# Kernel tuning notes

Measured on AMD Instinct MI355X. Metric: run time of the kernel, lower is better.

## Reference

```python
import jax, jax.numpy as jnp
import numpy as np

TEMPERATURE = 0.07
N, D, NUM_CLASSES = 8192, 1024, 128


def setup_inputs() -> dict:
    key = jax.random.key(0)
    k1, k2 = jax.random.split(key)
    embeddings = jax.random.normal(k1, (N, D), dtype=jnp.float32)
    labels = jax.random.randint(k2, (N,), 0, NUM_CLASSES, dtype=jnp.int64)
    return {"embeddings": embeddings, "labels": labels}


def reference(embeddings, labels):
    # L2-normalize rows (eps matches F.normalize default clamp of 1e-12 on the norm)
    norm = jnp.maximum(jnp.linalg.norm(embeddings, axis=-1, keepdims=True), 1e-12)
    emb = embeddings / norm
    # [N, N] similarity scaled by temperature
    sim = jnp.matmul(emb, emb.T) / TEMPERATURE
    # positive mask: same label, diagonal zeroed
    pos_mask = (labels[:, None] == labels[None, :]).astype(sim.dtype)
    pos_mask = pos_mask * (1.0 - jnp.eye(sim.shape[0], dtype=sim.dtype))
    exp_sim = jnp.exp(sim)
    sum_exp = exp_sim.sum(axis=1)              # [N]
    pos_sum = (exp_sim * pos_mask).sum(axis=1)  # [N]
    loss = -jnp.log(pos_sum / sum_exp)
    return loss.mean()
```

## Files before the change

kernel.cpp:

```cpp
#include <hip/hip_runtime.h>
#include <hip/hip_bf16.h>
#include <math.h>

#define N 8192
#define D 1024
#define TILE 128
#define BK 32
#define NTILES (N / TILE)
#define NBLOCKS (NTILES * (NTILES + 1) / 2)

typedef __bf16 bf16_t;
typedef bf16_t bf16x4 __attribute__((ext_vector_type(4)));
typedef bf16_t bf16x8 __attribute__((ext_vector_type(8)));
typedef float f32x4 __attribute__((ext_vector_type(4)));

__global__ __launch_bounds__(256) void norm_cast(const float* __restrict__ in,
                                                 bf16_t* __restrict__ out) {
    const int row = blockIdx.x;
    const int tid = threadIdx.x;
    const float4 v = ((const float4*)(in + (size_t)row * D))[tid];
    float ss = v.x * v.x + v.y * v.y + v.z * v.z + v.w * v.w;
    #pragma unroll
    for (int off = 32; off >= 1; off >>= 1) ss += __shfl_xor(ss, off, 64);
    __shared__ float red[4];
    const int wave = tid >> 6, lane = tid & 63;
    if (lane == 0) red[wave] = ss;
    __syncthreads();
    const float tot = red[0] + red[1] + red[2] + red[3];
    const float scale = 1.0f / fmaxf(sqrtf(tot), 1e-12f);
    bf16x4 o;
    o[0] = (bf16_t)(v.x * scale);
    o[1] = (bf16_t)(v.y * scale);
    o[2] = (bf16_t)(v.z * scale);
    o[3] = (bf16_t)(v.w * scale);
    ((bf16x4*)(out + (size_t)row * D))[tid] = o;
}

__global__ __launch_bounds__(256) void gemm_fused(const bf16_t* __restrict__ E,
                                                  const int* __restrict__ labels,
                                                  float* __restrict__ sumExp,
                                                  float* __restrict__ posSum) {
    __shared__ bf16_t As[TILE * BK];
    __shared__ bf16_t Bs[TILE * BK];
    __shared__ int labR[TILE], labC[TILE];

    const int b = blockIdx.x;
    int ti = (int)((sqrtf(8.0f * (float)b + 1.0f) - 1.0f) * 0.5f);
    while ((ti + 1) * (ti + 2) / 2 <= b) ++ti;
    while (ti * (ti + 1) / 2 > b) --ti;
    const int tj = b - ti * (ti + 1) / 2;
    const bool isDiag = (ti == tj);

    const int tid     = threadIdx.x;
    const int wave    = tid >> 6;
    const int lane    = tid & 63;
    const int q       = lane >> 4;
    const int lr      = lane & 15;
    const int waveRow = wave >> 1;
    const int waveCol = wave & 1;
    const int rowStart = ti * TILE;
    const int colStart = tj * TILE;

    if (tid < TILE) labR[tid] = labels[rowStart + tid];
    else            labC[tid - TILE] = labels[colStart + (tid - TILE)];

    f32x4 acc[4][4];
    #pragma unroll
    for (int i = 0; i < 4; ++i)
        #pragma unroll
        for (int j = 0; j < 4; ++j)
            acc[i][j] = {0.f, 0.f, 0.f, 0.f};

    const char* baseA = (const char*)(E + (size_t)rowStart * D);
    const char* baseB = (const char*)(E + (size_t)colStart * D);

    const int runit = q ^ ((lr >> 1) & 3);

    for (int kk = 0; kk < D; kk += BK) {
        #pragma unroll
        for (int p = 0; p < 2; ++p) {
            const int u  = p * 256 + tid;
            const int r  = u >> 2;
            const int uc = (u & 3) ^ ((r >> 1) & 3);
            const char* ga = baseA + (size_t)r * (D * 2) + kk * 2 + uc * 16;
            const char* gb = baseB + (size_t)r * (D * 2) + kk * 2 + uc * 16;
            char* la = (char*)As + (p * 256 + wave * 64) * 16;
            char* lb = (char*)Bs + (p * 256 + wave * 64) * 16;
            __builtin_amdgcn_global_load_lds(
                (const __attribute__((address_space(1))) void*)ga,
                (__attribute__((address_space(3))) void*)la, 16, 0, 0);
            __builtin_amdgcn_global_load_lds(
                (const __attribute__((address_space(1))) void*)gb,
                (__attribute__((address_space(3))) void*)lb, 16, 0, 0);
        }
        __syncthreads();

        bf16x8 af[4], bfr[4];
        #pragma unroll
        for (int ri = 0; ri < 4; ++ri)
            af[ri] = *(const bf16x8*)((const char*)As +
                     (waveRow * 64 + ri * 16 + lr) * 64 + runit * 16);
        #pragma unroll
        for (int ci = 0; ci < 4; ++ci)
            bfr[ci] = *(const bf16x8*)((const char*)Bs +
                      (waveCol * 64 + ci * 16 + lr) * 64 + runit * 16);
        #pragma unroll
        for (int ri = 0; ri < 4; ++ri)
            #pragma unroll
            for (int ci = 0; ci < 4; ++ci)
                acc[ri][ci] = __builtin_amdgcn_mfma_f32_16x16x32_bf16(
                    af[ri], bfr[ci], acc[ri][ci], 0, 0, 0);
        __syncthreads();
    }

    const float invT = 1.0f / 0.07f;
    float colAll[4] = {0.f, 0.f, 0.f, 0.f};
    float colPos[4] = {0.f, 0.f, 0.f, 0.f};
    #pragma unroll
    for (int ri = 0; ri < 4; ++ri) {
        #pragma unroll
        for (int e = 0; e < 4; ++e) {
            const int rloc = waveRow * 64 + ri * 16 + q * 4 + e;
            const int gi   = rowStart + rloc;
            const int li   = labR[rloc];
            float s_all = 0.f, s_pos = 0.f;
            #pragma unroll
            for (int ci = 0; ci < 4; ++ci) {
                const int cloc = waveCol * 64 + ci * 16 + lr;
                const int gj   = colStart + cloc;
                const float v  = __expf(acc[ri][ci][e] * invT);
                const bool same = (labC[cloc] == li);
                s_all += v;
                if (same && gi != gj) s_pos += v;
                if (!isDiag) {
                    colAll[ci] += v;
                    if (same) colPos[ci] += v;
                }
            }
            #pragma unroll
            for (int off = 1; off < 16; off <<= 1) {
                s_all += __shfl_xor(s_all, off, 64);
                s_pos += __shfl_xor(s_pos, off, 64);
            }
            if (lr == 0) {
                atomicAdd(&sumExp[gi], s_all);
                atomicAdd(&posSum[gi], s_pos);
            }
        }
    }
    if (!isDiag) {
        #pragma unroll
        for (int ci = 0; ci < 4; ++ci) {
            float a = colAll[ci], p = colPos[ci];
            a += __shfl_xor(a, 16, 64);  a += __shfl_xor(a, 32, 64);
            p += __shfl_xor(p, 16, 64);  p += __shfl_xor(p, 32, 64);
            if (q == 0) {
                const int gj = colStart + waveCol * 64 + ci * 16 + lr;
                atomicAdd(&sumExp[gj], a);
                atomicAdd(&posSum[gj], p);
            }
        }
    }
}

__global__ __launch_bounds__(1024) void finalize(const float* __restrict__ sumExp,
                                                 const float* __restrict__ posSum,
                                                 float* __restrict__ out) {
    const int tid = threadIdx.x;
    float s = 0.f;
    #pragma unroll
    for (int i = tid; i < N; i += 1024)
        s += __logf(sumExp[i] / posSum[i]);
    #pragma unroll
    for (int off = 32; off >= 1; off >>= 1) s += __shfl_xor(s, off, 64);
    __shared__ float red[16];
    if ((tid & 63) == 0) red[tid >> 6] = s;
    __syncthreads();
    if (tid == 0) {
        float t = 0.f;
        #pragma unroll
        for (int i = 0; i < 16; ++i) t += red[i];
        out[0] = t / (float)N;
    }
}

extern "C" void kernel_launch(void* const* d_in, const int* in_sizes, int n_in,
                              void* d_out, int out_size, void* d_ws, size_t ws_size,
                              hipStream_t stream) {
    const float* emb    = (const float*)d_in[0];
    const int*   labels = (const int*)d_in[1];
    float* out = (float*)d_out;

    float*  sumExp = (float*)d_ws;
    float*  posSum = sumExp + N;
    bf16_t* EN     = (bf16_t*)((char*)d_ws + (size_t)2 * N * sizeof(float));

    hipMemsetAsync(d_ws, 0, (size_t)2 * N * sizeof(float), stream);

    norm_cast<<<N, 256, 0, stream>>>(emb, EN);

    gemm_fused<<<NBLOCKS, 256, 0, stream>>>(EN, labels, sumExp, posSum);

    finalize<<<1, 1024, 0, stream>>>(sumExp, posSum, out);
}
```

Measured before the change: 216.6 us.

## Rewrite fused GEMM with 256x256 tiles, double-buffered async LDS staging and phased MFMA schedule

The fused similarity GEMM moves from 128x128 tiles with a single-buffered BK=32 loop to 256x256 tiles with 512 threads and BK=64 double-buffered LDS. Global-to-LDS loads are interleaved with MFMA phases using explicit waitcnt, barriers and setprio, so that memory latency overlaps compute. Block indices are remapped in strides of 8 to spread tiles across the device. Labels are now read straight from global memory instead of through shared memory. The larger tiles raise data reuse, but they also raise register and LDS pressure, and 528 blocks may balance less evenly across the CUs.

```diff
diff --git a/kernel.cpp b/kernel.cpp
--- a/kernel.cpp
+++ b/kernel.cpp
@@ -4,10 +4,11 @@
 
 #define N 8192
 #define D 1024
-#define TILE 128
-#define BK 32
-#define NTILES (N / TILE)
-#define NBLOCKS (NTILES * (NTILES + 1) / 2)
+#define BM 256
+#define BK 64
+#define NTIL 32
+#define NBLK 528
+#define ITERS 8
 
 typedef __bf16 bf16_t;
 typedef bf16_t bf16x4 __attribute__((ext_vector_type(4)));
@@ -36,105 +37,205 @@
     ((bf16x4*)(out + (size_t)row * D))[tid] = o;
 }
 
-__global__ __launch_bounds__(256) void gemm_fused(const bf16_t* __restrict__ E,
-                                                  const int* __restrict__ labels,
-                                                  float* __restrict__ sumExp,
-                                                  float* __restrict__ posSum) {
-    __shared__ bf16_t As[TILE * BK];
-    __shared__ bf16_t Bs[TILE * BK];
-    __shared__ int labR[TILE], labC[TILE];
-
-    const int b = blockIdx.x;
+__global__ __launch_bounds__(512, 2) void gemm_fused(const bf16_t* __restrict__ E,
+                                                     const int* __restrict__ labels,
+                                                     float* __restrict__ sumExp,
+                                                     float* __restrict__ posSum) {
+    __shared__ bf16_t As[2][2][128 * 64];
+    __shared__ bf16_t Bs[2][2][128 * 64];
+
+    const int b0 = blockIdx.x;
+    const int b  = (b0 & 7) * (NBLK / 8) + (b0 >> 3);
+
     int ti = (int)((sqrtf(8.0f * (float)b + 1.0f) - 1.0f) * 0.5f);
     while ((ti + 1) * (ti + 2) / 2 <= b) ++ti;
     while (ti * (ti + 1) / 2 > b) --ti;
     const int tj = b - ti * (ti + 1) / 2;
     const bool isDiag = (ti == tj);
 
-    const int tid     = threadIdx.x;
-    const int wave    = tid >> 6;
-    const int lane    = tid & 63;
-    const int q       = lane >> 4;
-    const int lr      = lane & 15;
-    const int waveRow = wave >> 1;
-    const int waveCol = wave & 1;
-    const int rowStart = ti * TILE;
-    const int colStart = tj * TILE;
-
-    if (tid < TILE) labR[tid] = labels[rowStart + tid];
-    else            labC[tid - TILE] = labels[colStart + (tid - TILE)];
-
-    f32x4 acc[4][4];
-    #pragma unroll
-    for (int i = 0; i < 4; ++i)
+    const int tid  = threadIdx.x;
+    const int wave = tid >> 6;
+    const int lane = tid & 63;
+    const int lr   = lane & 15;
+    const int q    = lane >> 4;
+    const int wm   = wave >> 2;
+    const int wn   = wave & 3;
+    const int rowStart = ti * BM;
+    const int colStart = tj * BM;
+
+    f32x4 acc[8][4];
+    #pragma unroll
+    for (int m = 0; m < 8; ++m)
         #pragma unroll
-        for (int j = 0; j < 4; ++j)
-            acc[i][j] = {0.f, 0.f, 0.f, 0.f};
-
-    const char* baseA = (const char*)(E + (size_t)rowStart * D);
-    const char* baseB = (const char*)(E + (size_t)colStart * D);
-
-    const int runit = q ^ ((lr >> 1) & 3);
-
-    for (int kk = 0; kk < D; kk += BK) {
-        #pragma unroll
-        for (int p = 0; p < 2; ++p) {
-            const int u  = p * 256 + tid;
-            const int r  = u >> 2;
-            const int uc = (u & 3) ^ ((r >> 1) & 3);
-            const char* ga = baseA + (size_t)r * (D * 2) + kk * 2 + uc * 16;
-            const char* gb = baseB + (size_t)r * (D * 2) + kk * 2 + uc * 16;
-            char* la = (char*)As + (p * 256 + wave * 64) * 16;
-            char* lb = (char*)Bs + (p * 256 + wave * 64) * 16;
-            __builtin_amdgcn_global_load_lds(
-                (const __attribute__((address_space(1))) void*)ga,
-                (__attribute__((address_space(3))) void*)la, 16, 0, 0);
-            __builtin_amdgcn_global_load_lds(
-                (const __attribute__((address_space(1))) void*)gb,
-                (__attribute__((address_space(3))) void*)lb, 16, 0, 0);
+        for (int n = 0; n < 4; ++n) acc[m][n] = {0.f, 0.f, 0.f, 0.f};
+
+    const int r0  = tid >> 3;
+    const int lu0 = (tid & 7) ^ (r0 & 7);
+    const char* gA = (const char*)(E + (size_t)rowStart * D) + (size_t)r0 * (D * 2) + lu0 * 16;
+    const char* gB = (const char*)(E + (size_t)colStart * D) + (size_t)r0 * (D * 2) + lu0 * 16;
+
+    #define STAGE_A(buf, h, kb) do {                                                     \
+        const char* g0_ = gA + (size_t)(h) * (128 * 2048) + (kb);                        \
+        char* l0_ = (char*)&As[buf][h][0] + wave * 1024;                                 \
+        __builtin_amdgcn_global_load_lds((const __attribute__((address_space(1))) void*)g0_, \
+            (__attribute__((address_space(3))) void*)l0_, 16, 0, 0);                     \
+        __builtin_amdgcn_global_load_lds(                                                \
+            (const __attribute__((address_space(1))) void*)(g0_ + 64 * 2048),            \
+            (__attribute__((address_space(3))) void*)(l0_ + 8192), 16, 0, 0);            \
+    } while (0)
+    #define STAGE_B(buf, h, kb) do {                                                     \
+        const char* g0_ = gB + (size_t)(h) * (128 * 2048) + (kb);                        \
+        char* l0_ = (char*)&Bs[buf][h][0] + wave * 1024;                                 \
+        __builtin_amdgcn_global_load_lds((const __attribute__((address_space(1))) void*)g0_, \
+            (__attribute__((address_space(3))) void*)l0_, 16, 0, 0);                     \
+        __builtin_amdgcn_global_load_lds(                                                \
+            (const __attribute__((address_space(1))) void*)(g0_ + 64 * 2048),            \
+            (__attribute__((address_space(3))) void*)(l0_ + 8192), 16, 0, 0);            \
+    } while (0)
+
+    const int su0 = ((0 + q) ^ (lane & 7)) * 16;
+    const int su1 = ((4 + q) ^ (lane & 7)) * 16;
+    const char* rA0 = (const char*)&As[0][wm][0] + lr * 128;
+    const char* rA1 = (const char*)&As[1][wm][0] + lr * 128;
+    const char* rB0 = (const char*)&Bs[0][wn >> 1][0] + (wn & 1) * 8192 + lr * 128;
+    const char* rB1 = (const char*)&Bs[1][wn >> 1][0] + (wn & 1) * 8192 + lr * 128;
+
+    #define LD_A4(DST, RBASE, MOFFB, SU) do {                                            \
+        _Pragma("unroll")                                                                \
+        for (int m_ = 0; m_ < 4; ++m_)                                                   \
+            DST[m_] = *(const bf16x8*)((RBASE) + (MOFFB) + m_ * 2048 + (SU));            \
+    } while (0)
+    #define LD_B4(DST, RBASE, SU) do {                                                   \
+        _Pragma("unroll")                                                                \
+        for (int n_ = 0; n_ < 4; ++n_)                                                   \
+            DST[n_] = *(const bf16x8*)((RBASE) + n_ * 2048 + (SU));                      \
+    } while (0)
+    #define MFMA_QUAD(AF, BF, MO) do {                                                   \
+        _Pragma("unroll")                                                                \
+        for (int m_ = 0; m_ < 4; ++m_) {                                                 \
+            _Pragma("unroll")                                                            \
+            for (int n_ = 0; n_ < 4; ++n_)                                               \
+                acc[(MO) + m_][n_] = __builtin_amdgcn_mfma_f32_16x16x32_bf16(            \
+                    AF[m_], BF[n_], acc[(MO) + m_][n_], 0, 0, 0);                        \
+        }                                                                                \
+    } while (0)
+    #define PHASE_MID() do {                                                             \
+        __builtin_amdgcn_s_barrier();                                                    \
+        asm volatile("s_waitcnt lgkmcnt(0)");                                            \
+        __builtin_amdgcn_sched_barrier(0);                                               \
+        __builtin_amdgcn_s_setprio(1);                                                   \
+    } while (0)
+    #define PHASE_END() do {                                                             \
+        __builtin_amdgcn_s_setprio(0);                                                   \
+        __builtin_amdgcn_s_barrier();                                                    \
+    } while (0)
+
+    bf16x8 a0[4], a1[4], bq0[4], bq1[4];
+
+    STAGE_B(0, 0, 0);  STAGE_B(0, 1, 0);
+    STAGE_A(0, 0, 0);  STAGE_A(0, 1, 0);
+    STAGE_B(1, 0, 128); STAGE_B(1, 1, 128);
+    asm volatile("s_waitcnt vmcnt(4)" ::: "memory");
+    __builtin_amdgcn_sched_barrier(0);
+    __builtin_amdgcn_s_barrier();
+
+    #pragma unroll 1
+    for (int it = 0; it < ITERS; ++it) {
+        const bool lastIt = (it == ITERS - 1);
+        const int kb1 = (2 * it + 1) * 128;
+        const int kb2 = (2 * it + 2) * 128;
+        const int kb3 = (2 * it + 3) * 128;
+
+        LD_A4(a0, rA0, 0, su0);
+        LD_B4(bq0, rB0, su0);
+        STAGE_A(1, 0, kb1);
+        PHASE_MID();
+        MFMA_QUAD(a0, bq0, 0);
+        PHASE_END();
+
+        LD_A4(a1, rA0, 0, su1);
+        LD_B4(bq1, rB0, su1);
+        STAGE_A(1, 1, kb1);
+        PHASE_MID();
+        MFMA_QUAD(a1, bq1, 0);
+        PHASE_END();
+
+        LD_A4(a0, rA0, 8192, su0);
+        if (!lastIt) STAGE_B(0, 0, kb2);
+        PHASE_MID();
+        MFMA_QUAD(a0, bq0, 4);
+        PHASE_END();
+
+        LD_A4(a1, rA0, 8192, su1);
+        if (!lastIt) {
+            STAGE_B(0, 1, kb2);
+            asm volatile("s_waitcnt vmcnt(4)" ::: "memory");
+        } else {
+            asm volatile("s_waitcnt vmcnt(0)" ::: "memory");
         }
-        __syncthreads();
-
-        bf16x8 af[4], bfr[4];
-        #pragma unroll
-        for (int ri = 0; ri < 4; ++ri)
-            af[ri] = *(const bf16x8*)((const char*)As +
-                     (waveRow * 64 + ri * 16 + lr) * 64 + runit * 16);
-        #pragma unroll
-        for (int ci = 0; ci < 4; ++ci)
-            bfr[ci] = *(const bf16x8*)((const char*)Bs +
-                      (waveCol * 64 + ci * 16 + lr) * 64 + runit * 16);
-        #pragma unroll
-        for (int ri = 0; ri < 4; ++ri)
-            #pragma unroll
-            for (int ci = 0; ci < 4; ++ci)
-                acc[ri][ci] = __builtin_amdgcn_mfma_f32_16x16x32_bf16(
-                    af[ri], bfr[ci], acc[ri][ci], 0, 0, 0);
-        __syncthreads();
+        __builtin_amdgcn_sched_barrier(0);
+        PHASE_MID();
+        MFMA_QUAD(a1, bq1, 4);
+        PHASE_END();
+
+        LD_A4(a0, rA1, 0, su0);
+        LD_B4(bq0, rB1, su0);
+        if (!lastIt) STAGE_A(0, 0, kb2);
+        PHASE_MID();
+        MFMA_QUAD(a0, bq0, 0);
+        PHASE_END();
+
+        LD_A4(a1, rA1, 0, su1);
+        LD_B4(bq1, rB1, su1);
+        if (!lastIt) STAGE_A(0, 1, kb2);
+        PHASE_MID();
+        MFMA_QUAD(a1, bq1, 0);
+        PHASE_END();
+
+        LD_A4(a0, rA1, 8192, su0);
+        if (!lastIt) STAGE_B(1, 0, kb3);
+        PHASE_MID();
+        MFMA_QUAD(a0, bq0, 4);
+        PHASE_END();
+
+        LD_A4(a1, rA1, 8192, su1);
+        if (!lastIt) {
+            STAGE_B(1, 1, kb3);
+            asm volatile("s_waitcnt vmcnt(4)" ::: "memory");
+            __builtin_amdgcn_sched_barrier(0);
+        }
+        PHASE_MID();
+        MFMA_QUAD(a1, bq1, 4);
+        PHASE_END();
     }
 
     const float invT = 1.0f / 0.07f;
+    int lc[4];
+    #pragma unroll
+    for (int n = 0; n < 4; ++n)
+        lc[n] = labels[colStart + wn * 64 + n * 16 + lr];
+
     float colAll[4] = {0.f, 0.f, 0.f, 0.f};
     float colPos[4] = {0.f, 0.f, 0.f, 0.f};
     #pragma unroll
-    for (int ri = 0; ri < 4; ++ri) {
+    for (int m = 0; m < 8; ++m) {
         #pragma unroll
         for (int e = 0; e < 4; ++e) {
-            const int rloc = waveRow * 64 + ri * 16 + q * 4 + e;
+            const int rloc = wm * 128 + m * 16 + q * 4 + e;
             const int gi   = rowStart + rloc;
-            const int li   = labR[rloc];
+            const int li   = labels[gi];
             float s_all = 0.f, s_pos = 0.f;
             #pragma unroll
-            for (int ci = 0; ci < 4; ++ci) {
-                const int cloc = waveCol * 64 + ci * 16 + lr;
+            for (int n = 0; n < 4; ++n) {
+                const int cloc = wn * 64 + n * 16 + lr;
                 const int gj   = colStart + cloc;
-                const float v  = __expf(acc[ri][ci][e] * invT);
-                const bool same = (labC[cloc] == li);
+                const float v  = __expf(acc[m][n][e] * invT);
+                const bool same = (lc[n] == li);
                 s_all += v;
                 if (same && gi != gj) s_pos += v;
                 if (!isDiag) {
-                    colAll[ci] += v;
-                    if (same) colPos[ci] += v;
+                    colAll[n] += v;
+                    if (same) colPos[n] += v;
                 }
             }
             #pragma unroll
@@ -150,12 +251,12 @@
     }
     if (!isDiag) {
         #pragma unroll
-        for (int ci = 0; ci < 4; ++ci) {
-            float a = colAll[ci], p = colPos[ci];
+        for (int n = 0; n < 4; ++n) {
+            float a = colAll[n], p = colPos[n];
             a += __shfl_xor(a, 16, 64);  a += __shfl_xor(a, 32, 64);
             p += __shfl_xor(p, 16, 64);  p += __shfl_xor(p, 32, 64);
             if (q == 0) {
-                const int gj = colStart + waveCol * 64 + ci * 16 + lr;
+                const int gj = colStart + wn * 64 + n * 16 + lr;
                 atomicAdd(&sumExp[gj], a);
                 atomicAdd(&posSum[gj], p);
             }
@@ -199,7 +300,7 @@
 
     norm_cast<<<N, 256, 0, stream>>>(emb, EN);
 
-    gemm_fused<<<NBLOCKS, 256, 0, stream>>>(EN, labels, sumExp, posSum);
+    gemm_fused<<<NBLK, 512, 0, stream>>>(EN, labels, sumExp, posSum);
 
     finalize<<<1, 1024, 0, stream>>>(sumExp, posSum, out);
 }
```

Measured after the change: 219.2 us. About the same (+1.2%).
